# Kernel optimization log

Hardware: AMD Instinct MI355X
Metric: run time of the kernel (lower is better)

The kernel has to match this reference:

```python
import jax, jax.numpy as jnp
import numpy as np

N, E, F, H = 20000, 320000, 128, 256   # nodes, edges, in-features, hidden
M, NQ = 4096, 2048                      # lsq rows, QP variables
LAMB_MAX = 2.0


def setup_inputs() -> dict:
    key = jax.random.key(0)
    ks = jax.random.split(key, 12)
    x = jax.random.normal(ks[0], (N, F), jnp.float32)
    edge_index = jax.random.randint(ks[1], (2, E), 0, N)
    A = jax.random.normal(ks[2], (M, NQ), jnp.float32) * 0.05
    b = jax.random.normal(ks[3], (M, 1), jnp.float32)
    feat_ids = jax.random.randint(ks[4], (NQ,), 0, N)
    x_prior = jax.random.uniform(ks[5], (NQ, 1), jnp.float32)
    lamb = jnp.ones((1,), jnp.float32)
    # ChebConv K=2 weights: one linear per Chebyshev order, plus bias
    W10 = jax.random.normal(ks[6], (F, H), jnp.float32) / np.sqrt(F)
    W11 = jax.random.normal(ks[7], (F, H), jnp.float32) / np.sqrt(F)
    b1 = jnp.zeros((H,), jnp.float32)
    W20 = jax.random.normal(ks[8], (H, 1), jnp.float32) / np.sqrt(H)
    W21 = jax.random.normal(ks[9], (H, 1), jnp.float32) / np.sqrt(H)
    b2 = jnp.zeros((1,), jnp.float32)
    return {"x": x, "edge_index": edge_index, "A": A, "b": b,
            "feat_ids": feat_ids, "x_prior": x_prior, "lamb": lamb,
            "W10": W10, "W11": W11, "b1": b1,
            "W20": W20, "W21": W21, "b2": b2}


def _cheb_conv(x, edge_index, W0, W1, bias, lam_max):
    """PyG ChebConv with K=2: out = x @ W0 + (2L/lam_max - I) x @ W1 + bias,
    L = I - D^{-1/2} A D^{-1/2}, via edge gather/scatter (no dense NxN)."""
    row, col = edge_index[0], edge_index[1]
    n = x.shape[0]
    deg = jax.ops.segment_sum(jnp.ones_like(row, dtype=x.dtype), row, num_segments=n)
    dinv = jnp.where(deg > 0, deg ** -0.5, 0.0)
    # normalized edge weight scaled by 2/lam_max, negated (off-diag of L_hat)
    w = -(2.0 / lam_max) * dinv[row] * dinv[col]              # [E]
    msg = jax.ops.segment_sum(w[:, None] * x[col], row, num_segments=n)
    Tx1 = msg + (2.0 / lam_max - 1.0) * x                      # diagonal of L_hat
    return x @ W0 + Tx1 @ W1 + bias


def reference(x, edge_index, A, b, feat_ids, x_prior, lamb,
              W10, W11, b1, W20, W21, b2):
    h = jax.nn.relu(_cheb_conv(x, edge_index, W10, W11, b1, LAMB_MAX))
    h = lamb[0] * jax.nn.relu(_cheb_conv(h, edge_index, W20, W21, b2, LAMB_MAX))
    hfold = h[feat_ids] + 1e-5                                 # [NQ, 1]
    q = hfold[:, 0]
    # QP: min 1/2 z^T Q z + p^T z with vacuous inequality (0*z <= 0.1) and no
    # equality constraints -> interior-point converges to unconstrained min.
    Q = A.T @ A + jnp.diag(q)                                  # [NQ, NQ]
    p = -(x_prior * hfold)[:, 0] - (b.T @ A)[0]                # [NQ]
    z = jnp.linalg.solve(Q, -p)                                # [NQ]
    return z[:, None]                                          # f.T -> [NQ, 1]
```

## Files before the change

kernel.cpp:

```cpp
#include <hip/hip_runtime.h>

#define N_NODES 20000
#define N_EDGES 320000
#define F_DIM   128
#define H_DIM   256
#define M_ROWS  4096
#define NQ      2048
#define NIT     18
#define MM_ROWS 20032

typedef __attribute__((ext_vector_type(8))) short short8;
typedef __attribute__((ext_vector_type(4))) float f32x4;


__device__ __forceinline__ float wred(float v) {
#pragma unroll
  for (int m = 32; m > 0; m >>= 1) v += __shfl_xor(v, m, 64);
  return v;
}

__device__ __forceinline__ float bred256(float v, float* lds) {
  v = wred(v);
  int w = threadIdx.x >> 6;
  if ((threadIdx.x & 63) == 0) lds[w] = v;
  __syncthreads();
  float tot = lds[0] + lds[1] + lds[2] + lds[3];
  __syncthreads();
  return tot;
}

__device__ __forceinline__ unsigned f2bf(float f) {
  unsigned u = __float_as_uint(f);
  unsigned r = u + 0x7fffu + ((u >> 16) & 1u);
  return r >> 16;
}
__device__ __forceinline__ float bflo(unsigned u) { return __uint_as_float(u << 16); }
__device__ __forceinline__ float bfhi(unsigned u) { return __uint_as_float(u & 0xffff0000u); }


__global__ __launch_bounds__(1024) void k_scan(const int* __restrict__ deg,
    int* __restrict__ rowstart, float* __restrict__ dinv) {
  __shared__ int part[1024];
  int t = threadIdx.x;
  const int chunk = (N_NODES + 1023) / 1024;
  int lo = t * chunk;
  int hi = lo + chunk; if (hi > N_NODES) hi = N_NODES;
  int s = 0;
  for (int i = lo; i < hi; ++i) {
    int d = deg[i];
    dinv[i] = d > 0 ? rsqrtf((float)d) : 0.f;
    s += d;
  }
  part[t] = s;
  __syncthreads();
  for (int off = 1; off < 1024; off <<= 1) {
    int v = part[t];
    int add = (t >= off) ? part[t - off] : 0;
    __syncthreads();
    part[t] = v + add;
    __syncthreads();
  }
  int base = (t > 0) ? part[t - 1] : 0;
  for (int i = lo; i < hi; ++i) { rowstart[i] = base; base += deg[i]; }
  if (t == 0) rowstart[N_NODES] = part[1023];
}

__global__ __launch_bounds__(256) void k_scatter(const int* __restrict__ ei,
    const int* __restrict__ rowstart, int* __restrict__ cursor,
    const float* __restrict__ dinv, int* __restrict__ cols, float* __restrict__ wvals) {
  int e = blockIdx.x * 256 + threadIdx.x;
  if (e >= N_EDGES) return;
  int r = ei[e];
  int c = ei[N_EDGES + e];
  int pos = rowstart[r] + atomicAdd(&cursor[r], 1);
  cols[pos] = c;
  wvals[pos] = -dinv[r] * dinv[c];
}

#define CONVX_BLKS (MM_ROWS * 16 / 256)
#define DEG_BLKS   ((N_EDGES + 255) / 256)

__global__ __launch_bounds__(256) void k_pack(const float* __restrict__ x,
    const float* __restrict__ W10, const float* __restrict__ W11,
    unsigned* __restrict__ xu, unsigned* __restrict__ Wtb,
    const int* __restrict__ ei, int* __restrict__ deg) {
  int bx = blockIdx.x;
  if (bx < CONVX_BLKS) {
    int gid = bx * 256 + threadIdx.x;
    int row = gid >> 4;
    int q8 = gid & 15;
    uint4* xu4 = (uint4*)xu;
    if (row < N_NODES) {
      const float4* x4 = (const float4*)x;
      float4 a = x4[(size_t)row * 32 + q8 * 2];
      float4 b = x4[(size_t)row * 32 + q8 * 2 + 1];
      uint4 u;
      u.x = f2bf(a.x) | (f2bf(a.y) << 16);
      u.y = f2bf(a.z) | (f2bf(a.w) << 16);
      u.z = f2bf(b.x) | (f2bf(b.y) << 16);
      u.w = f2bf(b.z) | (f2bf(b.w) << 16);
      xu4[(size_t)row * 32 + q8] = u;
    } else {
      uint4 z = make_uint4(0, 0, 0, 0);
      xu4[(size_t)row * 32 + q8] = z;
      xu4[(size_t)row * 32 + 16 + q8] = z;
    }
  } else if (bx < CONVX_BLKS + 128) {
    int gid = (bx - CONVX_BLKS) * 256 + threadIdx.x;
    int n = gid >> 7;
    int u = gid & 127;
    int k0 = u * 2;
    float v0 = (k0 < 128) ? W10[(size_t)k0 * H_DIM + n]
                          : W11[(size_t)(k0 - 128) * H_DIM + n];
    float v1 = (k0 + 1 < 128) ? W10[(size_t)(k0 + 1) * H_DIM + n]
                              : W11[(size_t)(k0 - 127) * H_DIM + n];
    Wtb[(size_t)n * 128 + u] = f2bf(v0) | (f2bf(v1) << 16);
  } else {
    int e = (bx - CONVX_BLKS - 128) * 256 + threadIdx.x;
    if (e < N_EDGES) atomicAdd(&deg[ei[e]], 1);
  }
}

#define MSG_BLKS (N_NODES / 4)

__global__ __launch_bounds__(256) void k_msgprep(const int* __restrict__ rowstart,
    const int* __restrict__ cols, const float* __restrict__ wvals,
    unsigned* __restrict__ xu,
    const float* __restrict__ A, const float* __restrict__ b,
    unsigned* __restrict__ Atu, float* __restrict__ btA_parts) {
  const int bid = blockIdx.x;
  if (bid < MSG_BLKS) {
    int wid = (bid * 256 + threadIdx.x) >> 6;
    int lane = threadIdx.x & 63;
    if (wid >= N_NODES) return;
    int s0 = rowstart[wid], s1 = rowstart[wid + 1];
    float2 acc = make_float2(0.f, 0.f);
    for (int e = s0; e < s1; ++e) {
      int c = cols[e];
      float w = wvals[e];
      unsigned u = xu[(size_t)c * 128 + lane];
      acc.x += w * bflo(u);
      acc.y += w * bfhi(u);
    }
    xu[(size_t)wid * 128 + 64 + lane] = f2bf(acc.x) | (f2bf(acc.y) << 16);
  } else {
    const int pb = bid - MSG_BLKS;
    int jp = (pb & 3) * 256 + threadIdx.x;
    int k0 = (pb >> 2) * 128;
    const float2* A2 = (const float2*)A;
    float acc0 = 0.f, acc1 = 0.f;
    for (int kk = 0; kk < 128; kk += 8) {
      float ax[8], ay[8];
#pragma unroll
      for (int i = 0; i < 8; ++i) {
        int k = k0 + kk + i;
        float2 a = A2[(size_t)k * 1024 + jp];
        float bk = b[k];
        acc0 += a.x * bk;
        acc1 += a.y * bk;
        ax[i] = a.x; ay[i] = a.y;
      }
      uint4 t0, t1;
      t0.x = f2bf(ax[0]) | (f2bf(ax[1]) << 16);
      t0.y = f2bf(ax[2]) | (f2bf(ax[3]) << 16);
      t0.z = f2bf(ax[4]) | (f2bf(ax[5]) << 16);
      t0.w = f2bf(ax[6]) | (f2bf(ax[7]) << 16);
      t1.x = f2bf(ay[0]) | (f2bf(ay[1]) << 16);
      t1.y = f2bf(ay[2]) | (f2bf(ay[3]) << 16);
      t1.z = f2bf(ay[4]) | (f2bf(ay[5]) << 16);
      t1.w = f2bf(ay[6]) | (f2bf(ay[7]) << 16);
      int uoff = (k0 + kk) >> 1;
      *(uint4*)(Atu + (size_t)(2 * jp) * 2048 + uoff) = t0;
      *(uint4*)(Atu + (size_t)(2 * jp + 1) * 2048 + uoff) = t1;
    }
    ((float2*)(btA_parts + (size_t)(pb >> 2) * NQ))[jp] = make_float2(acc0, acc1);
  }
}


__device__ __forceinline__ void mm_ldfrag(short8* Af, short8* Bf,
    const unsigned* __restrict__ xurow, const unsigned* __restrict__ wrow, int kc) {
#pragma unroll
  for (int a = 0; a < 4; ++a)
    Af[a] = *(const short8*)(xurow + (size_t)a * 16 * 128 + kc * 16);
#pragma unroll
  for (int n = 0; n < 4; ++n)
    Bf[n] = *(const short8*)(wrow + (size_t)n * 16 * 128 + kc * 16);
}

__global__ __launch_bounds__(256) void k_mm(const unsigned* __restrict__ xu,
    const unsigned* __restrict__ Wtb, const float* __restrict__ b1,
    const float* __restrict__ W20, const float* __restrict__ W21,
    float* __restrict__ t, float* __restrict__ s) {
  const int row0 = blockIdx.x * 64;
  const int tid = threadIdx.x;
  const int w = tid >> 6, lane = tid & 63;
  const int colb = w * 64;
  const int frow = lane & 15, fqo = (lane >> 4) * 4;
  const int c16 = lane & 15, q4 = lane >> 4;

  f32x4 acc[4][4];
#pragma unroll
  for (int a = 0; a < 4; ++a)
#pragma unroll
    for (int b = 0; b < 4; ++b) {
      acc[a][b][0] = 0.f; acc[a][b][1] = 0.f;
      acc[a][b][2] = 0.f; acc[a][b][3] = 0.f;
    }

  const unsigned* xurow = xu + (size_t)(row0 + frow) * 128 + fqo;
  const unsigned* wrow  = Wtb + (size_t)(colb + frow) * 128 + fqo;

  short8 A0[4], B0[4], A1[4], B1[4];
  mm_ldfrag(A0, B0, xurow, wrow, 0);
#pragma unroll
  for (int kp = 0; kp < 4; ++kp) {
    const int kc = kp * 2;
    mm_ldfrag(A1, B1, xurow, wrow, kc + 1);
#pragma unroll
    for (int a = 0; a < 4; ++a)
#pragma unroll
      for (int n = 0; n < 4; ++n)
        acc[a][n] = __builtin_amdgcn_mfma_f32_16x16x32_bf16(A0[a], B0[n], acc[a][n], 0, 0, 0);
    if (kc + 2 < 8) mm_ldfrag(A0, B0, xurow, wrow, kc + 2);
#pragma unroll
    for (int a = 0; a < 4; ++a)
#pragma unroll
      for (int n = 0; n < 4; ++n)
        acc[a][n] = __builtin_amdgcn_mfma_f32_16x16x32_bf16(A1[a], B1[n], acc[a][n], 0, 0, 0);
  }

  float tp[4][4] = {}, sp[4][4] = {};
#pragma unroll
  for (int b2 = 0; b2 < 4; ++b2) {
    int gc = colb + b2 * 16 + c16;
    float w20 = W20[gc], w21 = W21[gc], bb = b1[gc];
#pragma unroll
    for (int a = 0; a < 4; ++a)
#pragma unroll
      for (int r = 0; r < 4; ++r) {
        float val = acc[a][b2][r] + bb;
        val = val > 0.f ? val : 0.f;
        tp[a][r] += val * w20;
        sp[a][r] += val * w21;
      }
  }
#pragma unroll
  for (int a = 0; a < 4; ++a)
#pragma unroll
    for (int r = 0; r < 4; ++r) {
#pragma unroll
      for (int m = 1; m < 16; m <<= 1) {
        tp[a][r] += __shfl_xor(tp[a][r], m, 64);
        sp[a][r] += __shfl_xor(sp[a][r], m, 64);
      }
    }
  if (c16 == 0) {
#pragma unroll
    for (int a = 0; a < 4; ++a)
#pragma unroll
      for (int r = 0; r < 4; ++r) {
        int gr = row0 + a * 16 + q4 * 4 + r;
        if (gr < N_NODES) {
          atomicAdd(&t[gr], tp[a][r]);
          atomicAdd(&s[gr], sp[a][r]);
        }
      }
  }
}


__global__ __launch_bounds__(256) void k_h2(const float* __restrict__ t,
    const float* __restrict__ s, const int* __restrict__ rowstart,
    const int* __restrict__ cols, const float* __restrict__ wvals,
    const float* __restrict__ lamb, const float* __restrict__ b2, float* __restrict__ h2) {
  int i = blockIdx.x * 256 + threadIdx.x;
  if (i >= N_NODES) return;
  float m = 0.f;
  int s0 = rowstart[i], s1 = rowstart[i + 1];
  for (int e = s0; e < s1; ++e) m += wvals[e] * s[cols[e]];
  float val = t[i] + m + b2[0];
  val = val > 0.f ? val : 0.f;
  h2[i] = lamb[0] * val;
}

#define GR_ST2 36
#define NTILE 136

__global__ __launch_bounds__(512) void k_gram(const unsigned* __restrict__ Atu,
    float* __restrict__ Gp,
    const float* __restrict__ h2, const int* __restrict__ feat_ids,
    const float* __restrict__ x_prior, const float* __restrict__ btA_parts,
    float* __restrict__ q, float* __restrict__ r0) {
  if (blockIdx.x >= 544) {
    if (threadIdx.x < 256) {
      int j = (blockIdx.x - 544) * 256 + threadIdx.x;
      int f = feat_ids[j];
      float hf = h2[f] + 1e-5f;
      q[j] = hf;
      float bta = 0.f;
#pragma unroll
      for (int c = 0; c < 32; ++c) bta += btA_parts[(size_t)c * NQ + j];
      r0[j] = x_prior[j] * hf + bta;
    }
    return;
  }
  __shared__ unsigned shA[128 * GR_ST2];
  __shared__ unsigned shB[128 * GR_ST2];
  const int bid = blockIdx.x;
  const int wid = (bid & 7) * 68 + (bid >> 3);
  const int tile = wid >> 2;
  const int kq = wid & 3;
  int uu = tile, bi = 0;
  while (uu >= 16 - bi) { uu -= 16 - bi; ++bi; }
  const int bj = bi + uu;
  const int i0 = bi * 128, j0 = bj * 128;
  const int tid = threadIdx.x;
  const int w = tid >> 6, lane = tid & 63;
  const int wr = (w >> 2) * 64, wc = (w & 3) * 32;
  const int srow = tid >> 2, sua = (tid & 3) * 8;
  const int frow = lane & 15, fqo = (lane >> 4) * 4;

  f32x4 acc[4][2];
#pragma unroll
  for (int a = 0; a < 4; ++a)
#pragma unroll
    for (int b = 0; b < 2; ++b) {
      acc[a][b][0] = 0.f; acc[a][b][1] = 0.f;
      acc[a][b][2] = 0.f; acc[a][b][3] = 0.f;
    }

  const unsigned* pa = Atu + (size_t)(i0 + srow) * 2048 + kq * 512 + sua;
  const unsigned* pb = Atu + (size_t)(j0 + srow) * 2048 + kq * 512 + sua;

  uint4 pra0 = *(const uint4*)(pa);
  uint4 pra1 = *(const uint4*)(pa + 4);
  uint4 prb0 = *(const uint4*)(pb);
  uint4 prb1 = *(const uint4*)(pb + 4);

  unsigned* as = shA + srow * GR_ST2 + sua;
  unsigned* bs = shB + srow * GR_ST2 + sua;

  for (int sp = 0; sp < 16; ++sp) {
    *(uint4*)as = pra0; *(uint4*)(as + 4) = pra1;
    *(uint4*)bs = prb0; *(uint4*)(bs + 4) = prb1;
    if (sp + 1 < 16) {
      const int ku = (sp + 1) * 32;
      pra0 = *(const uint4*)(pa + ku);
      pra1 = *(const uint4*)(pa + ku + 4);
      prb0 = *(const uint4*)(pb + ku);
      prb1 = *(const uint4*)(pb + ku + 4);
    }
    __syncthreads();
#pragma unroll
    for (int kk = 0; kk < 2; ++kk) {
      short8 af[4], bf[2];
#pragma unroll
      for (int a = 0; a < 4; ++a)
        af[a] = *(const short8*)(shA + (wr + a * 16 + frow) * GR_ST2 + kk * 16 + fqo);
#pragma unroll
      for (int b2 = 0; b2 < 2; ++b2)
        bf[b2] = *(const short8*)(shB + (wc + b2 * 16 + frow) * GR_ST2 + kk * 16 + fqo);
#pragma unroll
      for (int a = 0; a < 4; ++a)
#pragma unroll
        for (int b2 = 0; b2 < 2; ++b2)
          acc[a][b2] = __builtin_amdgcn_mfma_f32_16x16x32_bf16(af[a], bf[b2], acc[a][b2], 0, 0, 0);
    }
    __syncthreads();
  }

  const int q4 = lane >> 4, c16 = lane & 15;
  float* Gz = Gp + ((size_t)kq * NTILE + tile) * 16384;
#pragma unroll
  for (int a = 0; a < 4; ++a)
#pragma unroll
    for (int b2 = 0; b2 < 2; ++b2)
#pragma unroll
      for (int r = 0; r < 4; ++r) {
        int lr = wr + a * 16 + q4 * 4 + r;
        int lc = wc + b2 * 16 + c16;
        Gz[lr * 128 + lc] = acc[a][b2][r];
      }
}

#define GT_ST 131

__global__ __launch_bounds__(256) void k_gconv(const float* __restrict__ Gp,
    const float* __restrict__ q, unsigned* __restrict__ Gb, float* __restrict__ qcorr) {
  __shared__ unsigned short T[128 * GT_ST];
  int uu = blockIdx.x, bi = 0;
  while (uu >= 16 - bi) { uu -= 16 - bi; ++bi; }
  const int bj = bi + uu;
  const int tid = threadIdx.x;
  const int r = tid >> 1, ch = (tid & 1) * 64;
  const size_t tile = (size_t)blockIdx.x * 16384;
  const float4* P0 = (const float4*)(Gp + tile + r * 128 + ch);
  const float4* P1 = (const float4*)(Gp + (size_t)1 * NTILE * 16384 + tile + r * 128 + ch);
  const float4* P2 = (const float4*)(Gp + (size_t)2 * NTILE * 16384 + tile + r * 128 + ch);
  const float4* P3 = (const float4*)(Gp + (size_t)3 * NTILE * 16384 + tile + r * 128 + ch);
  const int gr = bi * 128 + r;
  const bool hasdiag = (bi == bj) && (r >= ch) && (r < ch + 64);
  unsigned uo[32];
#pragma unroll
  for (int j = 0; j < 16; ++j) {
    float4 a = P0[j], b = P1[j], c = P2[j], d = P3[j];
    float v0 = a.x + b.x + c.x + d.x;
    float v1 = a.y + b.y + c.y + d.y;
    float v2 = a.z + b.z + c.z + d.z;
    float v3 = a.w + b.w + c.w + d.w;
    const int c0 = ch + j * 4;
    if (hasdiag && (r - c0 >= 0) && (r - c0 < 4)) {
      float qv = q[gr];
      int dsel = r - c0;
      if (dsel == 0) v0 += qv;
      else if (dsel == 1) v1 += qv;
      else if (dsel == 2) v2 += qv;
      else v3 += qv;
      float vd = (dsel == 0) ? v0 : (dsel == 1) ? v1 : (dsel == 2) ? v2 : v3;
      qcorr[gr] = vd - bflo(f2bf(vd));
    }
    unsigned u0 = f2bf(v0) | (f2bf(v1) << 16);
    unsigned u1 = f2bf(v2) | (f2bf(v3) << 16);
    uo[2 * j] = u0;
    uo[2 * j + 1] = u1;
    T[r * GT_ST + c0]     = (unsigned short)(u0 & 0xffffu);
    T[r * GT_ST + c0 + 1] = (unsigned short)(u0 >> 16);
    T[r * GT_ST + c0 + 2] = (unsigned short)(u1 & 0xffffu);
    T[r * GT_ST + c0 + 3] = (unsigned short)(u1 >> 16);
  }
  uint4* dst = (uint4*)(Gb + (size_t)gr * 1024 + bj * 64 + (ch >> 1));
#pragma unroll
  for (int j = 0; j < 8; ++j) dst[j] = ((const uint4*)uo)[j];
  __syncthreads();
  if (bi != bj) {
    const int wv = tid >> 6, lane = tid & 63;
    for (int kk = 0; kk < 32; ++kk) {
      int rr = kk * 4 + wv;
      unsigned lo = T[(2 * lane) * GT_ST + rr];
      unsigned hi = T[(2 * lane + 1) * GT_ST + rr];
      Gb[(size_t)(bj * 128 + rr) * 1024 + bi * 64 + lane] = lo | (hi << 16);
    }
  }
}

__global__ __launch_bounds__(256) void k_cgG(int k, const unsigned* __restrict__ Gb,
    const float* __restrict__ qcorr,
    const float* __restrict__ r_old, float* __restrict__ r_new,
    const float* __restrict__ p_old, float* __restrict__ p_new,
    const float* __restrict__ Qp_in, float* __restrict__ Qp_out,
    float* __restrict__ xcg) {
  __shared__ float pshare[NQ];
  __shared__ float lds[4];
  const int tid = threadIdx.x, bid = blockIdx.x;
  const float4* r4 = (const float4*)r_old;
  float4 ra = r4[tid * 2], rb2 = r4[tid * 2 + 1];
  float pv[8];
  if (k == 0) {
    pv[0] = ra.x; pv[1] = ra.y; pv[2] = ra.z; pv[3] = ra.w;
    pv[4] = rb2.x; pv[5] = rb2.y; pv[6] = rb2.z; pv[7] = rb2.w;
    if (bid == 0) {
      ((float4*)p_new)[tid * 2] = ra;
      ((float4*)p_new)[tid * 2 + 1] = rb2;
    }
  } else {
    const float4* p4 = (const float4*)p_old;
    const float4* qp4 = (const float4*)Qp_in;
    float4 pa = p4[tid * 2], pb = p4[tid * 2 + 1];
    float4 qa = qp4[tid * 2], qb = qp4[tid * 2 + 1];
    float rr = ra.x * ra.x + ra.y * ra.y + ra.z * ra.z + ra.w * ra.w +
               rb2.x * rb2.x + rb2.y * rb2.y + rb2.z * rb2.z + rb2.w * rb2.w;
    float pap = pa.x * qa.x + pa.y * qa.y + pa.z * qa.z + pa.w * qa.w +
                pb.x * qb.x + pb.y * qb.y + pb.z * qb.z + pb.w * qb.w;
    rr = bred256(rr, lds);
    pap = bred256(pap, lds);
    float alpha = rr / pap;
    if (bid == 0) {
      float4* x4 = (float4*)xcg;
      float4 xa = x4[tid * 2], xb = x4[tid * 2 + 1];
      xa.x += alpha * pa.x; xa.y += alpha * pa.y;
      xa.z += alpha * pa.z; xa.w += alpha * pa.w;
      xb.x += alpha * pb.x; xb.y += alpha * pb.y;
      xb.z += alpha * pb.z; xb.w += alpha * pb.w;
      x4[tid * 2] = xa; x4[tid * 2 + 1] = xb;
    }
    ra.x -= alpha * qa.x; ra.y -= alpha * qa.y;
    ra.z -= alpha * qa.z; ra.w -= alpha * qa.w;
    rb2.x -= alpha * qb.x; rb2.y -= alpha * qb.y;
    rb2.z -= alpha * qb.z; rb2.w -= alpha * qb.w;
    float rrn = ra.x * ra.x + ra.y * ra.y + ra.z * ra.z + ra.w * ra.w +
                rb2.x * rb2.x + rb2.y * rb2.y + rb2.z * rb2.z + rb2.w * rb2.w;
    rrn = bred256(rrn, lds);
    float beta = rrn / rr;
    pv[0] = ra.x + beta * pa.x; pv[1] = ra.y + beta * pa.y;
    pv[2] = ra.z + beta * pa.z; pv[3] = ra.w + beta * pa.w;
    pv[4] = rb2.x + beta * pb.x; pv[5] = rb2.y + beta * pb.y;
    pv[6] = rb2.z + beta * pb.z; pv[7] = rb2.w + beta * pb.w;
    if (bid == 0) {
      ((float4*)r_new)[tid * 2] = ra;
      ((float4*)r_new)[tid * 2 + 1] = rb2;
      ((float4*)p_new)[tid * 2] = make_float4(pv[0], pv[1], pv[2], pv[3]);
      ((float4*)p_new)[tid * 2 + 1] = make_float4(pv[4], pv[5], pv[6], pv[7]);
    }
  }
  ((float4*)pshare)[tid * 2] = make_float4(pv[0], pv[1], pv[2], pv[3]);
  ((float4*)pshare)[tid * 2 + 1] = make_float4(pv[4], pv[5], pv[6], pv[7]);
  __syncthreads();
  const int w = tid >> 6, lane = tid & 63;
  const int row0 = bid * 8 + w * 2;
  const uint4* Gr0 = (const uint4*)(Gb + (size_t)row0 * 1024);
  const uint4* Gr1 = (const uint4*)(Gb + (size_t)(row0 + 1) * 1024);
  const float4* ps4 = (const float4*)pshare;
  float acc0 = 0.f, acc1 = 0.f;
#pragma unroll
  for (int c = 0; c < 4; ++c) {
    uint4 g0 = Gr0[c * 64 + lane];
    uint4 g1 = Gr1[c * 64 + lane];
    float4 pa = ps4[c * 128 + lane * 2];
    float4 pb = ps4[c * 128 + lane * 2 + 1];
    acc0 += bflo(g0.x) * pa.x + bfhi(g0.x) * pa.y;
    acc0 += bflo(g0.y) * pa.z + bfhi(g0.y) * pa.w;
    acc0 += bflo(g0.z) * pb.x + bfhi(g0.z) * pb.y;
    acc0 += bflo(g0.w) * pb.z + bfhi(g0.w) * pb.w;
    acc1 += bflo(g1.x) * pa.x + bfhi(g1.x) * pa.y;
    acc1 += bflo(g1.y) * pa.z + bfhi(g1.y) * pa.w;
    acc1 += bflo(g1.z) * pb.x + bfhi(g1.z) * pb.y;
    acc1 += bflo(g1.w) * pb.z + bfhi(g1.w) * pb.w;
  }
  acc0 = wred(acc0);
  acc1 = wred(acc1);
  if (lane == 0) {
    Qp_out[row0] = acc0 + qcorr[row0] * pshare[row0];
    Qp_out[row0 + 1] = acc1 + qcorr[row0 + 1] * pshare[row0 + 1];
  }
}

__global__ __launch_bounds__(256) void k_cgfin(const float* __restrict__ r_last,
    const float* __restrict__ p_last, const float* __restrict__ Qp,
    const float* __restrict__ xcg, float* __restrict__ out) {
  const int tid = threadIdx.x;
  const int lane = tid & 63;
  const float4* r4 = (const float4*)r_last;
  const float4* p4 = (const float4*)p_last;
  const float4* q4 = (const float4*)Qp;
  float rr = 0.f, pap = 0.f;
#pragma unroll
  for (int c = 0; c < 4; ++c) {
#pragma unroll
    for (int hh = 0; hh < 2; ++hh) {
      float4 rv = r4[c * 128 + lane * 2 + hh];
      float4 pv = p4[c * 128 + lane * 2 + hh];
      float4 qv = q4[c * 128 + lane * 2 + hh];
      rr += rv.x * rv.x + rv.y * rv.y + rv.z * rv.z + rv.w * rv.w;
      pap += pv.x * qv.x + pv.y * qv.y + pv.z * qv.z + pv.w * qv.w;
    }
  }
  rr = wred(rr);
  pap = wred(pap);
  float alpha = rr / pap;
  const float4* x4 = (const float4*)xcg;
  float4* o4 = (float4*)out;
#pragma unroll
  for (int hh = 0; hh < 2; ++hh) {
    int i4 = tid * 2 + hh;
    float4 xv = x4[i4];
    float4 pv = p4[i4];
    xv.x += alpha * pv.x; xv.y += alpha * pv.y;
    xv.z += alpha * pv.z; xv.w += alpha * pv.w;
    o4[i4] = xv;
  }
}


extern "C" void kernel_launch(void* const* d_in, const int* in_sizes, int n_in,
                              void* d_out, int out_size, void* d_ws, size_t ws_size,
                              hipStream_t stream) {
  const float* x      = (const float*)d_in[0];
  const int*   ei     = (const int*)d_in[1];
  const float* A      = (const float*)d_in[2];
  const float* b      = (const float*)d_in[3];
  const int*   fids   = (const int*)d_in[4];
  const float* xprior = (const float*)d_in[5];
  const float* lamb   = (const float*)d_in[6];
  const float* W10    = (const float*)d_in[7];
  const float* W11    = (const float*)d_in[8];
  const float* b1     = (const float*)d_in[9];
  const float* W20    = (const float*)d_in[10];
  const float* W21    = (const float*)d_in[11];
  const float* b2     = (const float*)d_in[12];
  float* out = (float*)d_out;

  char* base = (char*)d_ws;
  size_t o = 0;
  auto alloc = [&](size_t bytes) { size_t r = o; o = (o + bytes + 255) & ~size_t(255); return r; };

  size_t off_deg    = alloc(N_NODES * 4);
  size_t off_cursor = alloc(N_NODES * 4);
  size_t off_xcg    = alloc(NQ * 4);
  size_t off_t      = alloc(N_NODES * 4);
  size_t off_s      = alloc(N_NODES * 4);
  size_t zero_end   = o;
  size_t off_rowst  = alloc((N_NODES + 1) * 4);
  size_t off_dinv   = alloc(N_NODES * 4);
  size_t off_h2     = alloc(N_NODES * 4);
  size_t off_q      = alloc(NQ * 4);
  size_t off_r0     = alloc(NQ * 4);
  size_t off_r1     = alloc(NQ * 4);
  size_t off_p0     = alloc(NQ * 4);
  size_t off_p1     = alloc(NQ * 4);
  size_t off_Qp0    = alloc(NQ * 4);
  size_t off_Qp1    = alloc(NQ * 4);
  size_t off_qcorr  = alloc(NQ * 4);
  size_t off_btAp   = alloc(32 * NQ * 4);
  size_t off_Wtb    = alloc(256 * 128 * 4);
  size_t sz_cols  = (size_t)N_EDGES * 4 + 256;
  size_t sz_wvals = (size_t)N_EDGES * 4 + 256;
  size_t sz_xmsg  = (size_t)MM_ROWS * 256 * 2;
  size_t union_gnn = sz_cols + sz_wvals + sz_xmsg;
  size_t sz_gb     = (size_t)NQ * NQ * 2;
  size_t off_union = alloc(union_gnn > sz_gb ? union_gnn : sz_gb);
  size_t off_atu   = alloc((size_t)M_ROWS * NQ * 2);
  size_t off_Gp    = alloc((size_t)4 * NTILE * 16384 * 4);
  if (o > ws_size) return;

  int*   deg      = (int*)(base + off_deg);
  int*   cursor   = (int*)(base + off_cursor);
  float* xcg      = (float*)(base + off_xcg);
  float* t        = (float*)(base + off_t);
  float* s        = (float*)(base + off_s);
  int*   rowstart = (int*)(base + off_rowst);
  float* dinv     = (float*)(base + off_dinv);
  float* h2       = (float*)(base + off_h2);
  float* q        = (float*)(base + off_q);
  float* rb[2]    = {(float*)(base + off_r0), (float*)(base + off_r1)};
  float* pg[2]    = {(float*)(base + off_p0), (float*)(base + off_p1)};
  float* Qpb[2]   = {(float*)(base + off_Qp0), (float*)(base + off_Qp1)};
  float* qcorr    = (float*)(base + off_qcorr);
  float* btA_parts = (float*)(base + off_btAp);
  unsigned* Wtb   = (unsigned*)(base + off_Wtb);
  int*   cols     = (int*)(base + off_union);
  float* wvals    = (float*)(base + off_union + sz_cols);
  unsigned* xmsgb = (unsigned*)(base + off_union + sz_cols + sz_wvals);
  unsigned* Gb    = (unsigned*)(base + off_union);
  unsigned* Atu   = (unsigned*)(base + off_atu);
  float* Gp       = (float*)(base + off_Gp);

  hipMemsetAsync(d_ws, 0, zero_end, stream);

  k_pack<<<CONVX_BLKS + 128 + DEG_BLKS, 256, 0, stream>>>(x, W10, W11, xmsgb, Wtb, ei, deg);
  k_scan<<<1, 1024, 0, stream>>>(deg, rowstart, dinv);
  k_scatter<<<DEG_BLKS, 256, 0, stream>>>(ei, rowstart, cursor, dinv, cols, wvals);

  k_msgprep<<<MSG_BLKS + 128, 256, 0, stream>>>(rowstart, cols, wvals, xmsgb,
                                                A, b, Atu, btA_parts);
  k_mm<<<MM_ROWS / 64, 256, 0, stream>>>(xmsgb, Wtb, b1, W20, W21, t, s);
  k_h2<<<(N_NODES + 255) / 256, 256, 0, stream>>>(t, s, rowstart, cols, wvals, lamb, b2, h2);

  k_gram<<<552, 512, 0, stream>>>(Atu, Gp, h2, fids, xprior, btA_parts, q, rb[0]);
  k_gconv<<<NTILE, 256, 0, stream>>>(Gp, q, Gb, qcorr);

  k_cgG<<<256, 256, 0, stream>>>(0, Gb, qcorr, rb[0], rb[0], pg[0], pg[0],
                                 Qpb[1], Qpb[0], xcg);
  for (int k = 1; k < NIT; ++k) {
    k_cgG<<<256, 256, 0, stream>>>(k, Gb, qcorr, rb[(k - 1) & 1], rb[k & 1],
                                   pg[(k - 1) & 1], pg[k & 1],
                                   Qpb[(k - 1) & 1], Qpb[k & 1], xcg);
  }
  k_cgfin<<<1, 256, 0, stream>>>(rb[(NIT - 1) & 1], pg[(NIT - 1) & 1],
                                 Qpb[(NIT - 1) & 1], xcg, out);
}
```

Measured before the change: 395.1 us.

## Move A-transpose prep into pack kernel and unroll edge gathers by four

The A^T bf16 packing and b^T A partial sums move from the message-passing kernel into the first pack kernel, which has no dependency on the graph CSR. That work can then overlap with the x packing and degree counting, and the message kernel shrinks to graph aggregation only. Both the first-layer message gather and the second-layer scalar gather are unrolled by four with independent accumulators to expose more memory-level parallelism. This changes the floating-point summation order slightly and makes the pack kernel heavier, which delays the k_scan launch.

Result: no change. 397.4 us (+0.6%).

```diff
diff --git a/kernel.cpp b/kernel.cpp
--- a/kernel.cpp
+++ b/kernel.cpp
@@ -79,11 +79,14 @@
 
 #define CONVX_BLKS (MM_ROWS * 16 / 256)
 #define DEG_BLKS   ((N_EDGES + 255) / 256)
+#define PREP_BASE  (CONVX_BLKS + 128 + DEG_BLKS)
 
 __global__ __launch_bounds__(256) void k_pack(const float* __restrict__ x,
     const float* __restrict__ W10, const float* __restrict__ W11,
     unsigned* __restrict__ xu, unsigned* __restrict__ Wtb,
-    const int* __restrict__ ei, int* __restrict__ deg) {
+    const int* __restrict__ ei, int* __restrict__ deg,
+    const float* __restrict__ A, const float* __restrict__ b,
+    unsigned* __restrict__ Atu, float* __restrict__ btA_parts) {
   int bx = blockIdx.x;
   if (bx < CONVX_BLKS) {
     int gid = bx * 256 + threadIdx.x;
@@ -93,12 +96,12 @@
     if (row < N_NODES) {
       const float4* x4 = (const float4*)x;
       float4 a = x4[(size_t)row * 32 + q8 * 2];
-      float4 b = x4[(size_t)row * 32 + q8 * 2 + 1];
+      float4 b2 = x4[(size_t)row * 32 + q8 * 2 + 1];
       uint4 u;
       u.x = f2bf(a.x) | (f2bf(a.y) << 16);
       u.y = f2bf(a.z) | (f2bf(a.w) << 16);
-      u.z = f2bf(b.x) | (f2bf(b.y) << 16);
-      u.w = f2bf(b.z) | (f2bf(b.w) << 16);
+      u.z = f2bf(b2.x) | (f2bf(b2.y) << 16);
+      u.w = f2bf(b2.z) | (f2bf(b2.w) << 16);
       xu4[(size_t)row * 32 + q8] = u;
     } else {
       uint4 z = make_uint4(0, 0, 0, 0);
@@ -115,36 +118,11 @@
     float v1 = (k0 + 1 < 128) ? W10[(size_t)(k0 + 1) * H_DIM + n]
                               : W11[(size_t)(k0 - 127) * H_DIM + n];
     Wtb[(size_t)n * 128 + u] = f2bf(v0) | (f2bf(v1) << 16);
-  } else {
+  } else if (bx < PREP_BASE) {
     int e = (bx - CONVX_BLKS - 128) * 256 + threadIdx.x;
     if (e < N_EDGES) atomicAdd(&deg[ei[e]], 1);
-  }
-}
-
-#define MSG_BLKS (N_NODES / 4)
-
-__global__ __launch_bounds__(256) void k_msgprep(const int* __restrict__ rowstart,
-    const int* __restrict__ cols, const float* __restrict__ wvals,
-    unsigned* __restrict__ xu,
-    const float* __restrict__ A, const float* __restrict__ b,
-    unsigned* __restrict__ Atu, float* __restrict__ btA_parts) {
-  const int bid = blockIdx.x;
-  if (bid < MSG_BLKS) {
-    int wid = (bid * 256 + threadIdx.x) >> 6;
-    int lane = threadIdx.x & 63;
-    if (wid >= N_NODES) return;
-    int s0 = rowstart[wid], s1 = rowstart[wid + 1];
-    float2 acc = make_float2(0.f, 0.f);
-    for (int e = s0; e < s1; ++e) {
-      int c = cols[e];
-      float w = wvals[e];
-      unsigned u = xu[(size_t)c * 128 + lane];
-      acc.x += w * bflo(u);
-      acc.y += w * bfhi(u);
-    }
-    xu[(size_t)wid * 128 + 64 + lane] = f2bf(acc.x) | (f2bf(acc.y) << 16);
   } else {
-    const int pb = bid - MSG_BLKS;
+    const int pb = bx - PREP_BASE;
     int jp = (pb & 3) * 256 + threadIdx.x;
     int k0 = (pb >> 2) * 128;
     const float2* A2 = (const float2*)A;
@@ -177,6 +155,39 @@
   }
 }
 
+__global__ __launch_bounds__(256) void k_msg1(const int* __restrict__ rowstart,
+    const int* __restrict__ cols, const float* __restrict__ wvals,
+    unsigned* __restrict__ xu) {
+  int wid = (blockIdx.x * 256 + threadIdx.x) >> 6;
+  int lane = threadIdx.x & 63;
+  if (wid >= N_NODES) return;
+  int s0 = rowstart[wid], s1 = rowstart[wid + 1];
+  float2 a0 = make_float2(0.f, 0.f), a1 = make_float2(0.f, 0.f);
+  float2 a2 = make_float2(0.f, 0.f), a3 = make_float2(0.f, 0.f);
+  int e = s0;
+  for (; e + 4 <= s1; e += 4) {
+    int c0 = cols[e], c1 = cols[e + 1], c2 = cols[e + 2], c3 = cols[e + 3];
+    float w0 = wvals[e], w1 = wvals[e + 1], w2 = wvals[e + 2], w3 = wvals[e + 3];
+    unsigned u0 = xu[(size_t)c0 * 128 + lane];
+    unsigned u1 = xu[(size_t)c1 * 128 + lane];
+    unsigned u2 = xu[(size_t)c2 * 128 + lane];
+    unsigned u3 = xu[(size_t)c3 * 128 + lane];
+    a0.x += w0 * bflo(u0); a0.y += w0 * bfhi(u0);
+    a1.x += w1 * bflo(u1); a1.y += w1 * bfhi(u1);
+    a2.x += w2 * bflo(u2); a2.y += w2 * bfhi(u2);
+    a3.x += w3 * bflo(u3); a3.y += w3 * bfhi(u3);
+  }
+  for (; e < s1; ++e) {
+    int c = cols[e];
+    float w = wvals[e];
+    unsigned u = xu[(size_t)c * 128 + lane];
+    a0.x += w * bflo(u); a0.y += w * bfhi(u);
+  }
+  float ax = (a0.x + a1.x) + (a2.x + a3.x);
+  float ay = (a0.y + a1.y) + (a2.y + a3.y);
+  xu[(size_t)wid * 128 + 64 + lane] = f2bf(ax) | (f2bf(ay) << 16);
+}
+
 
 __device__ __forceinline__ void mm_ldfrag(short8* Af, short8* Bf,
     const unsigned* __restrict__ xurow, const unsigned* __restrict__ wrow, int kc) {
@@ -276,9 +287,19 @@
     const float* __restrict__ lamb, const float* __restrict__ b2, float* __restrict__ h2) {
   int i = blockIdx.x * 256 + threadIdx.x;
   if (i >= N_NODES) return;
-  float m = 0.f;
   int s0 = rowstart[i], s1 = rowstart[i + 1];
-  for (int e = s0; e < s1; ++e) m += wvals[e] * s[cols[e]];
+  float m0 = 0.f, m1 = 0.f, m2 = 0.f, m3 = 0.f;
+  int e = s0;
+  for (; e + 4 <= s1; e += 4) {
+    int c0 = cols[e], c1 = cols[e + 1], c2 = cols[e + 2], c3 = cols[e + 3];
+    float w0 = wvals[e], w1 = wvals[e + 1], w2 = wvals[e + 2], w3 = wvals[e + 3];
+    m0 += w0 * s[c0];
+    m1 += w1 * s[c1];
+    m2 += w2 * s[c2];
+    m3 += w3 * s[c3];
+  }
+  for (; e < s1; ++e) m0 += wvals[e] * s[cols[e]];
+  float m = (m0 + m1) + (m2 + m3);
   float val = t[i] + m + b2[0];
   val = val > 0.f ? val : 0.f;
   h2[i] = lamb[0] * val;
@@ -647,12 +668,12 @@
 
   hipMemsetAsync(d_ws, 0, zero_end, stream);
 
-  k_pack<<<CONVX_BLKS + 128 + DEG_BLKS, 256, 0, stream>>>(x, W10, W11, xmsgb, Wtb, ei, deg);
+  k_pack<<<PREP_BASE + 128, 256, 0, stream>>>(x, W10, W11, xmsgb, Wtb, ei, deg,
+                                              A, b, Atu, btA_parts);
   k_scan<<<1, 1024, 0, stream>>>(deg, rowstart, dinv);
   k_scatter<<<DEG_BLKS, 256, 0, stream>>>(ei, rowstart, cursor, dinv, cols, wvals);
 
-  k_msgprep<<<MSG_BLKS + 128, 256, 0, stream>>>(rowstart, cols, wvals, xmsgb,
-                                                A, b, Atu, btA_parts);
+  k_msg1<<<N_NODES / 4, 256, 0, stream>>>(rowstart, cols, wvals, xmsgb);
   k_mm<<<MM_ROWS / 64, 256, 0, stream>>>(xmsgb, Wtb, b1, W20, W21, t, s);
   k_h2<<<(N_NODES + 255) / 256, 256, 0, stream>>>(t, s, rowstart, cols, wvals, lamb, b2, h2);
 
```
